# Optimization experiments

Hardware: AMD Instinct MI355X
Metric: run time of the kernel (lower is better)

## Reference

```python
import jax, jax.numpy as jnp
import numpy as np

DIM = 256
HEADS = 8
WIN = 8
N = WIN * WIN          # 64 tokens per window
NW = 1024              # windows per image (256x256 map, 8x8 windows)
BATCH = 4
B_ = BATCH * NW        # 4096
HEAD_DIM = DIM // HEADS


def _relative_position_index():
    # identical to the torch buffer construction in WindowAttention.__init__
    coords = np.stack(np.meshgrid(np.arange(WIN), np.arange(WIN), indexing='ij'))  # [2,W,W]
    flat = coords.reshape(2, -1)                                # [2, N]
    rel = flat[:, :, None] - flat[:, None, :]                   # [2, N, N]
    rel = rel.transpose(1, 2, 0).copy()                         # [N, N, 2]
    rel[:, :, 0] += WIN - 1
    rel[:, :, 1] += WIN - 1
    rel[:, :, 0] *= 2 * WIN - 1
    return jnp.asarray(rel.sum(-1), dtype=jnp.int32)            # [N, N], values in [0, 225)


def setup_inputs() -> dict:
    key = jax.random.key(0)
    ks = jax.random.split(key, 9)
    std = 0.02
    return {
        'x': jax.random.normal(ks[0], (B_, N, DIM), dtype=jnp.float32),
        'mask': jax.random.normal(ks[1], (NW, N, N), dtype=jnp.float32),
        'w_q': jax.random.normal(ks[2], (DIM, DIM), dtype=jnp.float32) * std,
        'b_q': jnp.zeros((DIM,), dtype=jnp.float32),
        'w_kv': jax.random.normal(ks[3], (2 * DIM, DIM), dtype=jnp.float32) * std,
        'b_kv': jnp.zeros((2 * DIM,), dtype=jnp.float32),
        'bias_table': jax.random.normal(ks[4], ((2 * WIN - 1) ** 2, HEADS), dtype=jnp.float32) * std,
        'w_o': jax.random.normal(ks[5], (DIM, DIM), dtype=jnp.float32) * std,
        'b_o': jnp.zeros((DIM,), dtype=jnp.float32),
        'rp_index': _relative_position_index(),
    }


def reference(x, mask, w_q, b_q, w_kv, b_kv, bias_table, w_o, b_o, rp_index):
    Bw, n, c = x.shape
    h, d = HEADS, c // HEADS
    scale = d ** -0.5

    # linear QKV projection (LinearProjection with attn_kv=None)
    q = (x @ w_q.T + b_q).reshape(Bw, n, h, d).transpose(0, 2, 1, 3)      # [B_, H, N, D]
    kv = (x @ w_kv.T + b_kv).reshape(Bw, n, 2, h, d).transpose(2, 0, 3, 1, 4)
    k, v = kv[0], kv[1]                                                    # [B_, H, N, D]

    # scaled QK^T
    attn = jnp.einsum('bhnd,bhmd->bhnm', q * scale, k)                     # [B_, H, N, N]

    # gathered relative position bias (ratio = 1 since attn_kv is None)
    bias = bias_table[rp_index]                                            # [N, N, H]
    attn = attn + bias.transpose(2, 0, 1)[None]                            # broadcast over B_

    # per-window additive mask
    nW = mask.shape[0]
    attn = attn.reshape(Bw // nW, nW, h, n, n) + mask[None, :, None]
    attn = attn.reshape(Bw, h, n, n)

    attn = jax.nn.softmax(attn, axis=-1)

    out = jnp.einsum('bhnm,bhmd->bhnd', attn, v)                           # [B_, H, N, D]
    out = out.transpose(0, 2, 1, 3).reshape(Bw, n, c)
    return out @ w_o.T + b_o
```

## Files before the change

### kernel.cpp

```cpp
#include <hip/hip_runtime.h>
#include <hip/hip_bf16.h>
#include <stdint.h>

typedef __bf16 bf16_t;
typedef bf16_t bf16x8 __attribute__((ext_vector_type(8)));
typedef bf16_t bf16x4 __attribute__((ext_vector_type(4)));
typedef bf16_t bf16x2 __attribute__((ext_vector_type(2)));
typedef float f32x4 __attribute__((ext_vector_type(4)));
typedef uint32_t u32x4 __attribute__((ext_vector_type(4)));

#define WS_WKV_OFF 65536
#define WS_WO_OFF  196608
#define WS_B8_OFF  524288
#define QSCALE 0.17677669529663687f

__global__ __launch_bounds__(256) void prep_kernel(
    const float* __restrict__ wq, const float* __restrict__ wkv,
    const float* __restrict__ wo, const float* __restrict__ bt,
    const int* __restrict__ rp,
    bf16_t* __restrict__ wsq, bf16_t* __restrict__ wskv,
    bf16_t* __restrict__ wso, float* __restrict__ bias8) {
  int t = blockIdx.x * 256 + threadIdx.x;
  if (t < 65536)  wsq[t]  = (bf16_t)(wq[t] * QSCALE);
  if (t < 131072) wskv[t] = (bf16_t)wkv[t];
  if (t < 65536)  wso[t]  = (bf16_t)wo[t];
  if (t < 4096) {
    int idx = rp[t];
#pragma unroll
    for (int h = 0; h < 8; ++h) bias8[h * 4096 + t] = bt[idx * 8 + h];
  }
}

__device__ __forceinline__ bf16x8 xpose_frag(uint32_t e0, uint32_t e1,
                                             uint32_t o0, uint32_t o1,
                                             int ad0, int ad1, bool hi) {
  uint32_t v0e = (uint32_t)__builtin_amdgcn_ds_bpermute(ad0, (int)e0);
  uint32_t v0o = (uint32_t)__builtin_amdgcn_ds_bpermute(ad0, (int)o0);
  uint32_t v1e = (uint32_t)__builtin_amdgcn_ds_bpermute(ad0, (int)e1);
  uint32_t v1o = (uint32_t)__builtin_amdgcn_ds_bpermute(ad0, (int)o1);
  uint32_t v2e = (uint32_t)__builtin_amdgcn_ds_bpermute(ad1, (int)e0);
  uint32_t v2o = (uint32_t)__builtin_amdgcn_ds_bpermute(ad1, (int)o0);
  uint32_t v3e = (uint32_t)__builtin_amdgcn_ds_bpermute(ad1, (int)e1);
  uint32_t v3o = (uint32_t)__builtin_amdgcn_ds_bpermute(ad1, (int)o1);
  u32x4 r;
  r.x = hi ? v0o : v0e;
  r.y = hi ? v1o : v1e;
  r.z = hi ? v2o : v2e;
  r.w = hi ? v3o : v3e;
  return __builtin_bit_cast(bf16x8, r);
}

__device__ __forceinline__ uint32_t pk2(float a, float b) {
  bf16x2 t = {(bf16_t)a, (bf16_t)b};
  return __builtin_bit_cast(uint32_t, t);
}

__global__ __launch_bounds__(512, 4) void win_attn_kernel(
    const float* __restrict__ x, const float* __restrict__ mask,
    const float* __restrict__ bq, const float* __restrict__ bkv,
    const float* __restrict__ bo,
    const bf16_t* __restrict__ wsq, const bf16_t* __restrict__ wskv,
    const bf16_t* __restrict__ wso, const float* __restrict__ bias8,
    float* __restrict__ out) {
  __shared__ bf16_t lds[35328];
  const int b    = blockIdx.x;
  const int tid  = threadIdx.x;
  const int h    = tid >> 6;
  const int lane = tid & 63;
  const int lrow = lane & 15;
  const int lgrp = lane >> 4;
  const bool hi  = (lgrp & 2) != 0;
  const int ad0  = ((((2 * lgrp) & 3) << 4) + lrow) << 2;
  const int ad1  = ((((2 * lgrp + 1) & 3) << 4) + lrow) << 2;
  const f32x4 zf = {0.f, 0.f, 0.f, 0.f};

  {
    const float4* xv = (const float4*)(x + (size_t)b * 16384);
#pragma unroll
    for (int j = 0; j < 8; ++j) {
      int i4 = j * 512 + tid;
      float4 v = xv[i4];
      int e = i4 * 4;
      int r = e >> 8, c = e & 255;
      bf16x4 w = {(bf16_t)v.x, (bf16_t)v.y, (bf16_t)v.z, (bf16_t)v.w};
      *(bf16x4*)(lds + r * 264 + c) = w;
    }
  }
  __syncthreads();

  bf16_t* ldsVt = lds + 16896 + h * 2304;

  {
    const bf16_t* WVh = wskv + (256 + h * 32) * 256;
    float bv0 = bkv[256 + h * 32 + lrow];
    float bv1 = bkv[256 + h * 32 + 16 + lrow];
#pragma unroll
    for (int vh = 0; vh < 2; ++vh) {
      f32x4 av[2][2];
      av[0][0] = av[0][1] = av[1][0] = av[1][1] = zf;
#pragma unroll
      for (int ks = 0; ks < 8; ++ks) {
        bf16x8 xa[2];
#pragma unroll
        for (int i = 0; i < 2; ++i)
          xa[i] = *(const bf16x8*)(lds + ((vh * 2 + i) * 16 + lrow) * 264 + ks * 32 + lgrp * 8);
        bf16x8 wvf[2];
#pragma unroll
        for (int tn = 0; tn < 2; ++tn)
          wvf[tn] = *(const bf16x8*)(WVh + (tn * 16 + lrow) * 256 + ks * 32 + lgrp * 8);
#pragma unroll
        for (int i = 0; i < 2; ++i)
#pragma unroll
          for (int tn = 0; tn < 2; ++tn)
            av[i][tn] = __builtin_amdgcn_mfma_f32_16x16x32_bf16(xa[i], wvf[tn], av[i][tn], 0, 0, 0);
      }
#pragma unroll
      for (int i = 0; i < 2; ++i)
#pragma unroll
        for (int tn = 0; tn < 2; ++tn) {
          float bv = tn ? bv1 : bv0;
          bf16x4 vv;
#pragma unroll
          for (int r = 0; r < 4; ++r) vv[r] = (bf16_t)(av[i][tn][r] + bv);
          *(bf16x4*)(ldsVt + (tn * 16 + lrow) * 72 + (vh * 2 + i) * 16 + lgrp * 4) = vv;
        }
    }
  }

  bf16x8 qb[4], ka[4];
  {
    const bf16_t* WQh = wsq + h * 32 * 256;
#pragma unroll
    for (int qh = 0; qh < 2; ++qh) {
      f32x4 aq[2][2];
      aq[0][0] = aq[0][1] = aq[1][0] = aq[1][1] = zf;
#pragma unroll
      for (int ks = 0; ks < 8; ++ks) {
        bf16x8 xb[2];
#pragma unroll
        for (int i = 0; i < 2; ++i)
          xb[i] = *(const bf16x8*)(lds + ((qh * 2 + i) * 16 + lrow) * 264 + ks * 32 + lgrp * 8);
        bf16x8 wqf[2];
#pragma unroll
        for (int tm = 0; tm < 2; ++tm)
          wqf[tm] = *(const bf16x8*)(WQh + (tm * 16 + lrow) * 256 + ks * 32 + lgrp * 8);
#pragma unroll
        for (int tm = 0; tm < 2; ++tm)
#pragma unroll
          for (int i = 0; i < 2; ++i)
            aq[tm][i] = __builtin_amdgcn_mfma_f32_16x16x32_bf16(wqf[tm], xb[i], aq[tm][i], 0, 0, 0);
      }
      uint32_t pq[2][2][2];
#pragma unroll
      for (int tm = 0; tm < 2; ++tm) {
        float4 b4 = *(const float4*)(bq + h * 32 + tm * 16 + lgrp * 4);
#pragma unroll
        for (int i = 0; i < 2; ++i) {
          pq[tm][i][0] = pk2(aq[tm][i][0] + b4.x * QSCALE, aq[tm][i][1] + b4.y * QSCALE);
          pq[tm][i][1] = pk2(aq[tm][i][2] + b4.z * QSCALE, aq[tm][i][3] + b4.w * QSCALE);
        }
      }
#pragma unroll
      for (int i = 0; i < 2; ++i)
        qb[qh * 2 + i] = xpose_frag(pq[0][i][0], pq[0][i][1], pq[1][i][0], pq[1][i][1], ad0, ad1, hi);
    }
  }
  {
    const bf16_t* WKh = wskv + h * 32 * 256;
#pragma unroll
    for (int kh = 0; kh < 2; ++kh) {
      f32x4 ak2[2][2];
      ak2[0][0] = ak2[0][1] = ak2[1][0] = ak2[1][1] = zf;
#pragma unroll
      for (int ks = 0; ks < 8; ++ks) {
        bf16x8 xb[2];
#pragma unroll
        for (int i = 0; i < 2; ++i)
          xb[i] = *(const bf16x8*)(lds + ((kh * 2 + i) * 16 + lrow) * 264 + ks * 32 + lgrp * 8);
        bf16x8 wkf[2];
#pragma unroll
        for (int tm = 0; tm < 2; ++tm)
          wkf[tm] = *(const bf16x8*)(WKh + (tm * 16 + lrow) * 256 + ks * 32 + lgrp * 8);
#pragma unroll
        for (int tm = 0; tm < 2; ++tm)
#pragma unroll
          for (int i = 0; i < 2; ++i)
            ak2[tm][i] = __builtin_amdgcn_mfma_f32_16x16x32_bf16(wkf[tm], xb[i], ak2[tm][i], 0, 0, 0);
      }
      uint32_t pk[2][2][2];
#pragma unroll
      for (int tm = 0; tm < 2; ++tm) {
        float4 k4 = *(const float4*)(bkv + h * 32 + tm * 16 + lgrp * 4);
#pragma unroll
        for (int i = 0; i < 2; ++i) {
          pk[tm][i][0] = pk2(ak2[tm][i][0] + k4.x, ak2[tm][i][1] + k4.y);
          pk[tm][i][1] = pk2(ak2[tm][i][2] + k4.z, ak2[tm][i][3] + k4.w);
        }
      }
#pragma unroll
      for (int i = 0; i < 2; ++i)
        ka[kh * 2 + i] = xpose_frag(pk[0][i][0], pk[0][i][1], pk[1][i][0], pk[1][i][1], ad0, ad1, hi);
    }
  }

  __syncthreads();

  const float* maskw = mask + (size_t)(b & 1023) * 4096;
  const float* biash = bias8 + h * 4096;
#pragma unroll
  for (int qt = 0; qt < 4; ++qt) {
    f32x4 st[4];
#pragma unroll
    for (int tm = 0; tm < 4; ++tm)
      st[tm] = __builtin_amdgcn_mfma_f32_16x16x32_bf16(ka[tm], qb[qt], zf, 0, 0, 0);
    int q = qt * 16 + lrow;
    float sm = 0.f;
#pragma unroll
    for (int tm = 0; tm < 4; ++tm) {
      int kb = tm * 16 + lgrp * 4;
      float4 mb = *(const float4*)(maskw + q * 64 + kb);
      float4 bb = *(const float4*)(biash + q * 64 + kb);
#pragma unroll
      for (int r = 0; r < 4; ++r) {
        float madd = (r == 0) ? (mb.x + bb.x) : (r == 1) ? (mb.y + bb.y)
                   : (r == 2) ? (mb.z + bb.z) : (mb.w + bb.w);
        float p = __expf(st[tm][r] + madd);
        st[tm][r] = p;
        sm += p;
      }
    }
    sm += __shfl_xor(sm, 16);
    sm += __shfl_xor(sm, 32);
    float rs = 1.0f / sm;
    uint32_t ppk[4][2];
#pragma unroll
    for (int tm = 0; tm < 4; ++tm) {
      ppk[tm][0] = pk2(st[tm][0] * rs, st[tm][1] * rs);
      ppk[tm][1] = pk2(st[tm][2] * rs, st[tm][3] * rs);
    }
    bf16x8 paf[2];
#pragma unroll
    for (int kf = 0; kf < 2; ++kf)
      paf[kf] = xpose_frag(ppk[2 * kf][0], ppk[2 * kf][1],
                           ppk[2 * kf + 1][0], ppk[2 * kf + 1][1], ad0, ad1, hi);
    f32x4 o[2] = {zf, zf};
#pragma unroll
    for (int dt = 0; dt < 2; ++dt)
#pragma unroll
      for (int kf = 0; kf < 2; ++kf) {
        bf16x8 vf = *(const bf16x8*)(ldsVt + (dt * 16 + lrow) * 72 + kf * 32 + lgrp * 8);
        o[dt] = __builtin_amdgcn_mfma_f32_16x16x32_bf16(paf[kf], vf, o[dt], 0, 0, 0);
      }
#pragma unroll
    for (int dt = 0; dt < 2; ++dt)
#pragma unroll
      for (int r = 0; r < 4; ++r)
        lds[(qt * 16 + lgrp * 4 + r) * 264 + h * 32 + dt * 16 + lrow] = (bf16_t)o[dt][r];
  }
  __syncthreads();

  const int nb = h * 32;
  float* outw = out + (size_t)b * 16384;
#pragma unroll
  for (int half = 0; half < 2; ++half) {
    f32x4 oc[2][2];
#pragma unroll
    for (int tm = 0; tm < 2; ++tm)
#pragma unroll
      for (int tn = 0; tn < 2; ++tn) oc[tm][tn] = zf;
#pragma unroll
    for (int ks = 0; ks < 8; ++ks) {
      bf16x8 ao[2];
#pragma unroll
      for (int tm = 0; tm < 2; ++tm)
        ao[tm] = *(const bf16x8*)(lds + ((half * 2 + tm) * 16 + lrow) * 264 + ks * 32 + lgrp * 8);
      bf16x8 bw[2];
#pragma unroll
      for (int tn = 0; tn < 2; ++tn)
        bw[tn] = *(const bf16x8*)(wso + (nb + tn * 16 + lrow) * 256 + ks * 32 + lgrp * 8);
#pragma unroll
      for (int tm = 0; tm < 2; ++tm)
#pragma unroll
        for (int tn = 0; tn < 2; ++tn)
          oc[tm][tn] = __builtin_amdgcn_mfma_f32_16x16x32_bf16(ao[tm], bw[tn], oc[tm][tn], 0, 0, 0);
    }
#pragma unroll
    for (int tn = 0; tn < 2; ++tn) {
      float bov = bo[nb + tn * 16 + lrow];
#pragma unroll
      for (int tm = 0; tm < 2; ++tm)
#pragma unroll
        for (int r = 0; r < 4; ++r)
          outw[((half * 2 + tm) * 16 + lgrp * 4 + r) * 256 + nb + tn * 16 + lrow] =
              oc[tm][tn][r] + bov;
    }
  }
}

extern "C" void kernel_launch(void* const* d_in, const int* in_sizes, int n_in,
                              void* d_out, int out_size, void* d_ws, size_t ws_size,
                              hipStream_t stream) {
  const float* x    = (const float*)d_in[0];
  const float* mask = (const float*)d_in[1];
  const float* wq   = (const float*)d_in[2];
  const float* bq   = (const float*)d_in[3];
  const float* wkv  = (const float*)d_in[4];
  const float* bkv  = (const float*)d_in[5];
  const float* bt   = (const float*)d_in[6];
  const float* wo   = (const float*)d_in[7];
  const float* bo   = (const float*)d_in[8];
  const int*   rp   = (const int*)d_in[9];
  float* out = (float*)d_out;

  bf16_t* wsq  = (bf16_t*)d_ws;
  bf16_t* wskv = wsq + WS_WKV_OFF;
  bf16_t* wso  = wsq + WS_WO_OFF;
  float*  bias8 = (float*)((char*)d_ws + WS_B8_OFF);

  prep_kernel<<<512, 256, 0, stream>>>(wq, wkv, wo, bt, rp, wsq, wskv, wso, bias8);

  win_attn_kernel<<<4096, 512, 0, stream>>>(
      x, mask, bq, bkv, bo, wsq, wskv, wso, bias8, out);
}
```

Measured before the change: 568.5 us.

## Split fused window attention into per-half-head attention and separate out-projection kernels

```diff
diff --git a/kernel.cpp b/kernel.cpp
--- a/kernel.cpp
+++ b/kernel.cpp
@@ -12,6 +12,8 @@
 #define WS_WKV_OFF 65536
 #define WS_WO_OFF  196608
 #define WS_B8_OFF  524288
+#define WS_O_OFF   1048576
+#define WS_NEEDED  (1048576ull + 134217728ull)
 #define QSCALE 0.17677669529663687f
 
 __global__ __launch_bounds__(256) void prep_kernel(
@@ -55,7 +57,260 @@
   return __builtin_bit_cast(uint32_t, t);
 }
 
-__global__ __launch_bounds__(512, 4) void win_attn_kernel(
+__global__ __launch_bounds__(256, 3) void attn_qkv_kernel(
+    const float* __restrict__ x, const float* __restrict__ mask,
+    const float* __restrict__ bq, const float* __restrict__ bkv,
+    const bf16_t* __restrict__ wsq, const bf16_t* __restrict__ wskv,
+    const float* __restrict__ bias8, bf16_t* __restrict__ Ob) {
+  __shared__ bf16_t lds[64 * 264];
+  const int wg   = blockIdx.x;
+  const int b    = wg >> 1;
+  const int half = wg & 1;
+  const int tid  = threadIdx.x;
+  const int h    = half * 4 + (tid >> 6);
+  const int lane = tid & 63;
+  const int lrow = lane & 15;
+  const int lgrp = lane >> 4;
+  const bool hi  = (lgrp & 2) != 0;
+  const int ad0  = ((((2 * lgrp) & 3) << 4) + lrow) << 2;
+  const int ad1  = ((((2 * lgrp + 1) & 3) << 4) + lrow) << 2;
+  const f32x4 zf = {0.f, 0.f, 0.f, 0.f};
+
+  {
+    const float4* xv = (const float4*)(x + (size_t)b * 16384);
+#pragma unroll
+    for (int j = 0; j < 16; ++j) {
+      int i4 = j * 256 + tid;
+      float4 v = xv[i4];
+      int e = i4 * 4;
+      int r = e >> 8, c = e & 255;
+      bf16x4 w = {(bf16_t)v.x, (bf16_t)v.y, (bf16_t)v.z, (bf16_t)v.w};
+      *(bf16x4*)(lds + r * 264 + c) = w;
+    }
+  }
+  __syncthreads();
+
+  bf16x8 vb[2][2];
+  {
+    const bf16_t* WVh = wskv + (256 + h * 32) * 256;
+    float bv0 = bkv[256 + h * 32 + lrow];
+    float bv1 = bkv[256 + h * 32 + 16 + lrow];
+#pragma unroll
+    for (int vh = 0; vh < 2; ++vh) {
+      f32x4 av[2][2];
+      av[0][0] = av[0][1] = av[1][0] = av[1][1] = zf;
+#pragma unroll
+      for (int ks = 0; ks < 8; ++ks) {
+        bf16x8 xa[2];
+#pragma unroll
+        for (int i = 0; i < 2; ++i)
+          xa[i] = *(const bf16x8*)(lds + ((vh * 2 + i) * 16 + lrow) * 264 + ks * 32 + lgrp * 8);
+        bf16x8 wvf[2];
+#pragma unroll
+        for (int tn = 0; tn < 2; ++tn)
+          wvf[tn] = *(const bf16x8*)(WVh + (tn * 16 + lrow) * 256 + ks * 32 + lgrp * 8);
+#pragma unroll
+        for (int i = 0; i < 2; ++i)
+#pragma unroll
+          for (int tn = 0; tn < 2; ++tn)
+            av[i][tn] = __builtin_amdgcn_mfma_f32_16x16x32_bf16(xa[i], wvf[tn], av[i][tn], 0, 0, 0);
+      }
+      uint32_t pkv[2][2][2];
+#pragma unroll
+      for (int i = 0; i < 2; ++i)
+#pragma unroll
+        for (int tn = 0; tn < 2; ++tn) {
+          float bv = tn ? bv1 : bv0;
+          pkv[i][tn][0] = pk2(av[i][tn][0] + bv, av[i][tn][1] + bv);
+          pkv[i][tn][1] = pk2(av[i][tn][2] + bv, av[i][tn][3] + bv);
+        }
+#pragma unroll
+      for (int dt = 0; dt < 2; ++dt)
+        vb[dt][vh] = xpose_frag(pkv[0][dt][0], pkv[0][dt][1],
+                                pkv[1][dt][0], pkv[1][dt][1], ad0, ad1, hi);
+    }
+  }
+
+  bf16x8 qb[4], ka[4];
+  {
+    const bf16_t* WQh = wsq + h * 32 * 256;
+#pragma unroll
+    for (int qh = 0; qh < 2; ++qh) {
+      f32x4 aq[2][2];
+      aq[0][0] = aq[0][1] = aq[1][0] = aq[1][1] = zf;
+#pragma unroll
+      for (int ks = 0; ks < 8; ++ks) {
+        bf16x8 xb[2];
+#pragma unroll
+        for (int i = 0; i < 2; ++i)
+          xb[i] = *(const bf16x8*)(lds + ((qh * 2 + i) * 16 + lrow) * 264 + ks * 32 + lgrp * 8);
+        bf16x8 wqf[2];
+#pragma unroll
+        for (int tm = 0; tm < 2; ++tm)
+          wqf[tm] = *(const bf16x8*)(WQh + (tm * 16 + lrow) * 256 + ks * 32 + lgrp * 8);
+#pragma unroll
+        for (int tm = 0; tm < 2; ++tm)
+#pragma unroll
+          for (int i = 0; i < 2; ++i)
+            aq[tm][i] = __builtin_amdgcn_mfma_f32_16x16x32_bf16(wqf[tm], xb[i], aq[tm][i], 0, 0, 0);
+      }
+      uint32_t pq[2][2][2];
+#pragma unroll
+      for (int tm = 0; tm < 2; ++tm) {
+        float4 b4 = *(const float4*)(bq + h * 32 + tm * 16 + lgrp * 4);
+#pragma unroll
+        for (int i = 0; i < 2; ++i) {
+          pq[tm][i][0] = pk2(aq[tm][i][0] + b4.x * QSCALE, aq[tm][i][1] + b4.y * QSCALE);
+          pq[tm][i][1] = pk2(aq[tm][i][2] + b4.z * QSCALE, aq[tm][i][3] + b4.w * QSCALE);
+        }
+      }
+#pragma unroll
+      for (int i = 0; i < 2; ++i)
+        qb[qh * 2 + i] = xpose_frag(pq[0][i][0], pq[0][i][1], pq[1][i][0], pq[1][i][1], ad0, ad1, hi);
+    }
+  }
+  {
+    const bf16_t* WKh = wskv + h * 32 * 256;
+#pragma unroll
+    for (int kh = 0; kh < 2; ++kh) {
+      f32x4 ak2[2][2];
+      ak2[0][0] = ak2[0][1] = ak2[1][0] = ak2[1][1] = zf;
+#pragma unroll
+      for (int ks = 0; ks < 8; ++ks) {
+        bf16x8 xb[2];
+#pragma unroll
+        for (int i = 0; i < 2; ++i)
+          xb[i] = *(const bf16x8*)(lds + ((kh * 2 + i) * 16 + lrow) * 264 + ks * 32 + lgrp * 8);
+        bf16x8 wkf[2];
+#pragma unroll
+        for (int tm = 0; tm < 2; ++tm)
+          wkf[tm] = *(const bf16x8*)(WKh + (tm * 16 + lrow) * 256 + ks * 32 + lgrp * 8);
+#pragma unroll
+        for (int tm = 0; tm < 2; ++tm)
+#pragma unroll
+          for (int i = 0; i < 2; ++i)
+            ak2[tm][i] = __builtin_amdgcn_mfma_f32_16x16x32_bf16(wkf[tm], xb[i], ak2[tm][i], 0, 0, 0);
+      }
+      uint32_t pkk[2][2][2];
+#pragma unroll
+      for (int tm = 0; tm < 2; ++tm) {
+        float4 k4 = *(const float4*)(bkv + h * 32 + tm * 16 + lgrp * 4);
+#pragma unroll
+        for (int i = 0; i < 2; ++i) {
+          pkk[tm][i][0] = pk2(ak2[tm][i][0] + k4.x, ak2[tm][i][1] + k4.y);
+          pkk[tm][i][1] = pk2(ak2[tm][i][2] + k4.z, ak2[tm][i][3] + k4.w);
+        }
+      }
+#pragma unroll
+      for (int i = 0; i < 2; ++i)
+        ka[kh * 2 + i] = xpose_frag(pkk[0][i][0], pkk[0][i][1], pkk[1][i][0], pkk[1][i][1], ad0, ad1, hi);
+    }
+  }
+
+  const float* maskw = mask + (size_t)(b & 1023) * 4096;
+  const float* biash = bias8 + h * 4096;
+  bf16_t* ow = Ob + (size_t)b * 16384 + h * 32;
+#pragma unroll
+  for (int qt = 0; qt < 4; ++qt) {
+    f32x4 st[4];
+#pragma unroll
+    for (int tm = 0; tm < 4; ++tm)
+      st[tm] = __builtin_amdgcn_mfma_f32_16x16x32_bf16(ka[tm], qb[qt], zf, 0, 0, 0);
+    int q = qt * 16 + lrow;
+    float sm = 0.f;
+#pragma unroll
+    for (int tm = 0; tm < 4; ++tm) {
+      int kb = tm * 16 + lgrp * 4;
+      float4 mb = *(const float4*)(maskw + q * 64 + kb);
+      float4 bb = *(const float4*)(biash + q * 64 + kb);
+#pragma unroll
+      for (int r = 0; r < 4; ++r) {
+        float madd = (r == 0) ? (mb.x + bb.x) : (r == 1) ? (mb.y + bb.y)
+                   : (r == 2) ? (mb.z + bb.z) : (mb.w + bb.w);
+        float p = __expf(st[tm][r] + madd);
+        st[tm][r] = p;
+        sm += p;
+      }
+    }
+    sm += __shfl_xor(sm, 16);
+    sm += __shfl_xor(sm, 32);
+    float rs = 1.0f / sm;
+    uint32_t ppk[4][2];
+#pragma unroll
+    for (int tm = 0; tm < 4; ++tm) {
+      ppk[tm][0] = pk2(st[tm][0] * rs, st[tm][1] * rs);
+      ppk[tm][1] = pk2(st[tm][2] * rs, st[tm][3] * rs);
+    }
+    bf16x8 paf[2];
+#pragma unroll
+    for (int kf = 0; kf < 2; ++kf)
+      paf[kf] = xpose_frag(ppk[2 * kf][0], ppk[2 * kf][1],
+                           ppk[2 * kf + 1][0], ppk[2 * kf + 1][1], ad0, ad1, hi);
+    f32x4 o[2] = {zf, zf};
+#pragma unroll
+    for (int dt = 0; dt < 2; ++dt)
+#pragma unroll
+      for (int kf = 0; kf < 2; ++kf)
+        o[dt] = __builtin_amdgcn_mfma_f32_16x16x32_bf16(paf[kf], vb[dt][kf], o[dt], 0, 0, 0);
+#pragma unroll
+    for (int dt = 0; dt < 2; ++dt)
+#pragma unroll
+      for (int r = 0; r < 4; ++r)
+        ow[(qt * 16 + lgrp * 4 + r) * 256 + dt * 16 + lrow] = (bf16_t)o[dt][r];
+  }
+}
+
+__global__ __launch_bounds__(256, 2) void outproj_kernel(
+    const bf16_t* __restrict__ Ob, const bf16_t* __restrict__ wso,
+    const float* __restrict__ bo, float* __restrict__ out) {
+  __shared__ bf16_t ldsA[64 * 264];
+  const int blk  = blockIdx.x;
+  const size_t t0 = (size_t)blk * 64;
+  const int tid  = threadIdx.x;
+  const int w    = tid >> 6;
+  const int lane = tid & 63;
+  const int lrow = lane & 15;
+  const int lgrp = lane >> 4;
+  const f32x4 zf = {0.f, 0.f, 0.f, 0.f};
+
+  {
+    const bf16_t* src = Ob + t0 * 256;
+#pragma unroll
+    for (int j = 0; j < 8; ++j) {
+      int idx = j * 256 + tid;
+      int e = idx * 8;
+      int r = e >> 8, c = e & 255;
+      *(bf16x8*)(ldsA + r * 264 + c) = *(const bf16x8*)(src + e);
+    }
+  }
+  __syncthreads();
+
+  float* outw = out + t0 * 256;
+#pragma unroll
+  for (int cp = 0; cp < 4; ++cp) {
+    f32x4 acc[4];
+#pragma unroll
+    for (int tn = 0; tn < 4; ++tn) acc[tn] = zf;
+#pragma unroll
+    for (int ks = 0; ks < 8; ++ks) {
+      bf16x8 ao = *(const bf16x8*)(ldsA + (w * 16 + lrow) * 264 + ks * 32 + lgrp * 8);
+#pragma unroll
+      for (int tn = 0; tn < 4; ++tn) {
+        bf16x8 bw = *(const bf16x8*)(wso + (cp * 64 + tn * 16 + lrow) * 256 + ks * 32 + lgrp * 8);
+        acc[tn] = __builtin_amdgcn_mfma_f32_16x16x32_bf16(ao, bw, acc[tn], 0, 0, 0);
+      }
+    }
+#pragma unroll
+    for (int tn = 0; tn < 4; ++tn) {
+      float bov = bo[cp * 64 + tn * 16 + lrow];
+#pragma unroll
+      for (int r = 0; r < 4; ++r)
+        outw[(w * 16 + lgrp * 4 + r) * 256 + cp * 64 + tn * 16 + lrow] = acc[tn][r] + bov;
+    }
+  }
+}
+
+__global__ __launch_bounds__(512, 2) void win_attn_fused(
     const float* __restrict__ x, const float* __restrict__ mask,
     const float* __restrict__ bq, const float* __restrict__ bkv,
     const float* __restrict__ bo,
@@ -73,7 +328,6 @@
   const int ad0  = ((((2 * lgrp) & 3) << 4) + lrow) << 2;
   const int ad1  = ((((2 * lgrp + 1) & 3) << 4) + lrow) << 2;
   const f32x4 zf = {0.f, 0.f, 0.f, 0.f};
-
   {
     const float4* xv = (const float4*)(x + (size_t)b * 16384);
 #pragma unroll
@@ -87,9 +341,7 @@
     }
   }
   __syncthreads();
-
   bf16_t* ldsVt = lds + 16896 + h * 2304;
-
   {
     const bf16_t* WVh = wskv + (256 + h * 32) * 256;
     float bv0 = bkv[256 + h * 32 + lrow];
@@ -126,85 +378,86 @@
         }
     }
   }
-
   bf16x8 qb[4], ka[4];
   {
     const bf16_t* WQh = wsq + h * 32 * 256;
-#pragma unroll
-    for (int qh = 0; qh < 2; ++qh) {
-      f32x4 aq[2][2];
-      aq[0][0] = aq[0][1] = aq[1][0] = aq[1][1] = zf;
-#pragma unroll
-      for (int ks = 0; ks < 8; ++ks) {
-        bf16x8 xb[2];
-#pragma unroll
-        for (int i = 0; i < 2; ++i)
-          xb[i] = *(const bf16x8*)(lds + ((qh * 2 + i) * 16 + lrow) * 264 + ks * 32 + lgrp * 8);
-        bf16x8 wqf[2];
-#pragma unroll
-        for (int tm = 0; tm < 2; ++tm)
-          wqf[tm] = *(const bf16x8*)(WQh + (tm * 16 + lrow) * 256 + ks * 32 + lgrp * 8);
-#pragma unroll
-        for (int tm = 0; tm < 2; ++tm)
-#pragma unroll
-          for (int i = 0; i < 2; ++i)
-            aq[tm][i] = __builtin_amdgcn_mfma_f32_16x16x32_bf16(wqf[tm], xb[i], aq[tm][i], 0, 0, 0);
-      }
-      uint32_t pq[2][2][2];
-#pragma unroll
-      for (int tm = 0; tm < 2; ++tm) {
-        float4 b4 = *(const float4*)(bq + h * 32 + tm * 16 + lgrp * 4);
-#pragma unroll
-        for (int i = 0; i < 2; ++i) {
-          pq[tm][i][0] = pk2(aq[tm][i][0] + b4.x * QSCALE, aq[tm][i][1] + b4.y * QSCALE);
-          pq[tm][i][1] = pk2(aq[tm][i][2] + b4.z * QSCALE, aq[tm][i][3] + b4.w * QSCALE);
-        }
-      }
-#pragma unroll
-      for (int i = 0; i < 2; ++i)
-        qb[qh * 2 + i] = xpose_frag(pq[0][i][0], pq[0][i][1], pq[1][i][0], pq[1][i][1], ad0, ad1, hi);
-    }
+    f32x4 aq[2][4];
+#pragma unroll
+    for (int tm = 0; tm < 2; ++tm)
+#pragma unroll
+      for (int tn = 0; tn < 4; ++tn) aq[tm][tn] = zf;
+#pragma unroll
+    for (int ks = 0; ks < 8; ++ks) {
+      bf16x8 xb[4];
+#pragma unroll
+      for (int tn = 0; tn < 4; ++tn)
+        xb[tn] = *(const bf16x8*)(lds + (tn * 16 + lrow) * 264 + ks * 32 + lgrp * 8);
+      bf16x8 wqf[2];
+#pragma unroll
+      for (int tm = 0; tm < 2; ++tm)
+        wqf[tm] = *(const bf16x8*)(WQh + (tm * 16 + lrow) * 256 + ks * 32 + lgrp * 8);
+#pragma unroll
+      for (int tm = 0; tm < 2; ++tm)
+#pragma unroll
+        for (int tn = 0; tn < 4; ++tn)
+          aq[tm][tn] = __builtin_amdgcn_mfma_f32_16x16x32_bf16(wqf[tm], xb[tn], aq[tm][tn], 0, 0, 0);
+    }
+    uint32_t pkq[2][4][2];
+#pragma unroll
+    for (int tm = 0; tm < 2; ++tm) {
+      float4 b4 = *(const float4*)(bq + h * 32 + tm * 16 + lgrp * 4);
+      float bqa[4] = {b4.x * QSCALE, b4.y * QSCALE, b4.z * QSCALE, b4.w * QSCALE};
+#pragma unroll
+      for (int tn = 0; tn < 4; ++tn)
+#pragma unroll
+        for (int pr = 0; pr < 2; ++pr)
+          pkq[tm][tn][pr] = pk2(aq[tm][tn][2 * pr] + bqa[2 * pr],
+                                aq[tm][tn][2 * pr + 1] + bqa[2 * pr + 1]);
+    }
+#pragma unroll
+    for (int t = 0; t < 4; ++t)
+      qb[t] = xpose_frag(pkq[0][t][0], pkq[0][t][1], pkq[1][t][0], pkq[1][t][1], ad0, ad1, hi);
   }
   {
     const bf16_t* WKh = wskv + h * 32 * 256;
-#pragma unroll
-    for (int kh = 0; kh < 2; ++kh) {
-      f32x4 ak2[2][2];
-      ak2[0][0] = ak2[0][1] = ak2[1][0] = ak2[1][1] = zf;
-#pragma unroll
-      for (int ks = 0; ks < 8; ++ks) {
-        bf16x8 xb[2];
-#pragma unroll
-        for (int i = 0; i < 2; ++i)
-          xb[i] = *(const bf16x8*)(lds + ((kh * 2 + i) * 16 + lrow) * 264 + ks * 32 + lgrp * 8);
-        bf16x8 wkf[2];
-#pragma unroll
-        for (int tm = 0; tm < 2; ++tm)
-          wkf[tm] = *(const bf16x8*)(WKh + (tm * 16 + lrow) * 256 + ks * 32 + lgrp * 8);
-#pragma unroll
-        for (int tm = 0; tm < 2; ++tm)
-#pragma unroll
-          for (int i = 0; i < 2; ++i)
-            ak2[tm][i] = __builtin_amdgcn_mfma_f32_16x16x32_bf16(wkf[tm], xb[i], ak2[tm][i], 0, 0, 0);
-      }
-      uint32_t pk[2][2][2];
-#pragma unroll
-      for (int tm = 0; tm < 2; ++tm) {
-        float4 k4 = *(const float4*)(bkv + h * 32 + tm * 16 + lgrp * 4);
-#pragma unroll
-        for (int i = 0; i < 2; ++i) {
-          pk[tm][i][0] = pk2(ak2[tm][i][0] + k4.x, ak2[tm][i][1] + k4.y);
-          pk[tm][i][1] = pk2(ak2[tm][i][2] + k4.z, ak2[tm][i][3] + k4.w);
-        }
-      }
-#pragma unroll
-      for (int i = 0; i < 2; ++i)
-        ka[kh * 2 + i] = xpose_frag(pk[0][i][0], pk[0][i][1], pk[1][i][0], pk[1][i][1], ad0, ad1, hi);
-    }
-  }
-
+    f32x4 akk[2][4];
+#pragma unroll
+    for (int tm = 0; tm < 2; ++tm)
+#pragma unroll
+      for (int tn = 0; tn < 4; ++tn) akk[tm][tn] = zf;
+#pragma unroll
+    for (int ks = 0; ks < 8; ++ks) {
+      bf16x8 xb[4];
+#pragma unroll
+      for (int tn = 0; tn < 4; ++tn)
+        xb[tn] = *(const bf16x8*)(lds + (tn * 16 + lrow) * 264 + ks * 32 + lgrp * 8);
+      bf16x8 wkf[2];
+#pragma unroll
+      for (int tm = 0; tm < 2; ++tm)
+        wkf[tm] = *(const bf16x8*)(WKh + (tm * 16 + lrow) * 256 + ks * 32 + lgrp * 8);
+#pragma unroll
+      for (int tm = 0; tm < 2; ++tm)
+#pragma unroll
+        for (int tn = 0; tn < 4; ++tn)
+          akk[tm][tn] = __builtin_amdgcn_mfma_f32_16x16x32_bf16(wkf[tm], xb[tn], akk[tm][tn], 0, 0, 0);
+    }
+    uint32_t pkk[2][4][2];
+#pragma unroll
+    for (int tm = 0; tm < 2; ++tm) {
+      float4 k4 = *(const float4*)(bkv + h * 32 + tm * 16 + lgrp * 4);
+      float bka[4] = {k4.x, k4.y, k4.z, k4.w};
+#pragma unroll
+      for (int tn = 0; tn < 4; ++tn)
+#pragma unroll
+        for (int pr = 0; pr < 2; ++pr)
+          pkk[tm][tn][pr] = pk2(akk[tm][tn][2 * pr] + bka[2 * pr],
+                                akk[tm][tn][2 * pr + 1] + bka[2 * pr + 1]);
+    }
+#pragma unroll
+    for (int t = 0; t < 4; ++t)
+      ka[t] = xpose_frag(pkk[0][t][0], pkk[0][t][1], pkk[1][t][0], pkk[1][t][1], ad0, ad1, hi);
+  }
   __syncthreads();
-
   const float* maskw = mask + (size_t)(b & 1023) * 4096;
   const float* biash = bias8 + h * 4096;
 #pragma unroll
@@ -258,7 +511,6 @@
         lds[(qt * 16 + lgrp * 4 + r) * 264 + h * 32 + dt * 16 + lrow] = (bf16_t)o[dt][r];
   }
   __syncthreads();
-
   const int nb = h * 32;
   float* outw = out + (size_t)b * 16384;
 #pragma unroll
@@ -316,9 +568,14 @@
   bf16_t* wskv = wsq + WS_WKV_OFF;
   bf16_t* wso  = wsq + WS_WO_OFF;
   float*  bias8 = (float*)((char*)d_ws + WS_B8_OFF);
+  bf16_t* Ob   = (bf16_t*)((char*)d_ws + WS_O_OFF);
 
   prep_kernel<<<512, 256, 0, stream>>>(wq, wkv, wo, bt, rp, wsq, wskv, wso, bias8);
 
-  win_attn_kernel<<<4096, 512, 0, stream>>>(
-      x, mask, bq, bkv, bo, wsq, wskv, wso, bias8, out);
-}
+  if (ws_size >= WS_NEEDED) {
+    attn_qkv_kernel<<<8192, 256, 0, stream>>>(x, mask, bq, bkv, wsq, wskv, bias8, Ob);
+    outproj_kernel<<<4096, 256, 0, stream>>>(Ob, wso, bo, out);
+  } else {
+    win_attn_fused<<<4096, 512, 0, stream>>>(x, mask, bq, bkv, bo, wsq, wskv, wso, bias8, out);
+  }
+}
```

Result: slower. 790.3 us (+39.0%).

## Use 256-thread blocks with two heads per wave and V kept in registers

Applied to the files above, without the earlier changes.

```diff
diff --git a/kernel.cpp b/kernel.cpp
--- a/kernel.cpp
+++ b/kernel.cpp
@@ -55,17 +55,17 @@
   return __builtin_bit_cast(uint32_t, t);
 }
 
-__global__ __launch_bounds__(512, 4) void win_attn_kernel(
+__global__ __launch_bounds__(256, 3) void win_attn_kernel(
     const float* __restrict__ x, const float* __restrict__ mask,
     const float* __restrict__ bq, const float* __restrict__ bkv,
     const float* __restrict__ bo,
     const bf16_t* __restrict__ wsq, const bf16_t* __restrict__ wskv,
     const bf16_t* __restrict__ wso, const float* __restrict__ bias8,
     float* __restrict__ out) {
-  __shared__ bf16_t lds[35328];
+  __shared__ bf16_t lds[64 * 264];
   const int b    = blockIdx.x;
   const int tid  = threadIdx.x;
-  const int h    = tid >> 6;
+  const int wid  = tid >> 6;
   const int lane = tid & 63;
   const int lrow = lane & 15;
   const int lgrp = lane >> 4;
@@ -77,8 +77,8 @@
   {
     const float4* xv = (const float4*)(x + (size_t)b * 16384);
 #pragma unroll
-    for (int j = 0; j < 8; ++j) {
-      int i4 = j * 512 + tid;
+    for (int j = 0; j < 16; ++j) {
+      int i4 = j * 256 + tid;
       float4 v = xv[i4];
       int e = i4 * 4;
       int r = e >> 8, c = e & 255;
@@ -88,211 +88,221 @@
   }
   __syncthreads();
 
-  bf16_t* ldsVt = lds + 16896 + h * 2304;
-
-  {
-    const bf16_t* WVh = wskv + (256 + h * 32) * 256;
-    float bv0 = bkv[256 + h * 32 + lrow];
-    float bv1 = bkv[256 + h * 32 + 16 + lrow];
-#pragma unroll
-    for (int vh = 0; vh < 2; ++vh) {
-      f32x4 av[2][2];
-      av[0][0] = av[0][1] = av[1][0] = av[1][1] = zf;
-#pragma unroll
-      for (int ks = 0; ks < 8; ++ks) {
-        bf16x8 xa[2];
+  const float* maskw = mask + (size_t)(b & 1023) * 4096;
+  uint32_t opk[2][4][4];
+
+#pragma unroll
+  for (int rd = 0; rd < 2; ++rd) {
+    const int h = wid + rd * 4;
+
+    bf16x8 vb[2][2];
+    {
+      const bf16_t* WVh = wskv + (256 + h * 32) * 256;
+      float bv0 = bkv[256 + h * 32 + lrow];
+      float bv1 = bkv[256 + h * 32 + 16 + lrow];
+#pragma unroll
+      for (int vh = 0; vh < 2; ++vh) {
+        f32x4 av[2][2];
+        av[0][0] = av[0][1] = av[1][0] = av[1][1] = zf;
+#pragma unroll
+        for (int ks = 0; ks < 8; ++ks) {
+          bf16x8 xa[2];
+#pragma unroll
+          for (int i = 0; i < 2; ++i)
+            xa[i] = *(const bf16x8*)(lds + ((vh * 2 + i) * 16 + lrow) * 264 + ks * 32 + lgrp * 8);
+          bf16x8 wvf[2];
+#pragma unroll
+          for (int tn = 0; tn < 2; ++tn)
+            wvf[tn] = *(const bf16x8*)(WVh + (tn * 16 + lrow) * 256 + ks * 32 + lgrp * 8);
+#pragma unroll
+          for (int i = 0; i < 2; ++i)
+#pragma unroll
+            for (int tn = 0; tn < 2; ++tn)
+              av[i][tn] = __builtin_amdgcn_mfma_f32_16x16x32_bf16(xa[i], wvf[tn], av[i][tn], 0, 0, 0);
+        }
+        uint32_t pkv[2][2][2];
 #pragma unroll
         for (int i = 0; i < 2; ++i)
-          xa[i] = *(const bf16x8*)(lds + ((vh * 2 + i) * 16 + lrow) * 264 + ks * 32 + lgrp * 8);
-        bf16x8 wvf[2];
-#pragma unroll
-        for (int tn = 0; tn < 2; ++tn)
-          wvf[tn] = *(const bf16x8*)(WVh + (tn * 16 + lrow) * 256 + ks * 32 + lgrp * 8);
+#pragma unroll
+          for (int tn = 0; tn < 2; ++tn) {
+            float bv = tn ? bv1 : bv0;
+            pkv[i][tn][0] = pk2(av[i][tn][0] + bv, av[i][tn][1] + bv);
+            pkv[i][tn][1] = pk2(av[i][tn][2] + bv, av[i][tn][3] + bv);
+          }
+#pragma unroll
+        for (int dt = 0; dt < 2; ++dt)
+          vb[dt][vh] = xpose_frag(pkv[0][dt][0], pkv[0][dt][1],
+                                  pkv[1][dt][0], pkv[1][dt][1], ad0, ad1, hi);
+      }
+    }
+
+    bf16x8 qb[4], ka[4];
+    {
+      const bf16_t* WQh = wsq + h * 32 * 256;
+#pragma unroll
+      for (int qh = 0; qh < 2; ++qh) {
+        f32x4 aq[2][2];
+        aq[0][0] = aq[0][1] = aq[1][0] = aq[1][1] = zf;
+#pragma unroll
+        for (int ks = 0; ks < 8; ++ks) {
+          bf16x8 xb[2];
+#pragma unroll
+          for (int i = 0; i < 2; ++i)
+            xb[i] = *(const bf16x8*)(lds + ((qh * 2 + i) * 16 + lrow) * 264 + ks * 32 + lgrp * 8);
+          bf16x8 wqf[2];
+#pragma unroll
+          for (int tm = 0; tm < 2; ++tm)
+            wqf[tm] = *(const bf16x8*)(WQh + (tm * 16 + lrow) * 256 + ks * 32 + lgrp * 8);
+#pragma unroll
+          for (int tm = 0; tm < 2; ++tm)
+#pragma unroll
+            for (int i = 0; i < 2; ++i)
+              aq[tm][i] = __builtin_amdgcn_mfma_f32_16x16x32_bf16(wqf[tm], xb[i], aq[tm][i], 0, 0, 0);
+        }
+        uint32_t pq[2][2][2];
+#pragma unroll
+        for (int tm = 0; tm < 2; ++tm) {
+          float4 b4 = *(const float4*)(bq + h * 32 + tm * 16 + lgrp * 4);
+#pragma unroll
+          for (int i = 0; i < 2; ++i) {
+            pq[tm][i][0] = pk2(aq[tm][i][0] + b4.x * QSCALE, aq[tm][i][1] + b4.y * QSCALE);
+            pq[tm][i][1] = pk2(aq[tm][i][2] + b4.z * QSCALE, aq[tm][i][3] + b4.w * QSCALE);
+          }
+        }
 #pragma unroll
         for (int i = 0; i < 2; ++i)
-#pragma unroll
-          for (int tn = 0; tn < 2; ++tn)
-            av[i][tn] = __builtin_amdgcn_mfma_f32_16x16x32_bf16(xa[i], wvf[tn], av[i][tn], 0, 0, 0);
-      }
-#pragma unroll
-      for (int i = 0; i < 2; ++i)
-#pragma unroll
-        for (int tn = 0; tn < 2; ++tn) {
-          float bv = tn ? bv1 : bv0;
-          bf16x4 vv;
-#pragma unroll
-          for (int r = 0; r < 4; ++r) vv[r] = (bf16_t)(av[i][tn][r] + bv);
-          *(bf16x4*)(ldsVt + (tn * 16 + lrow) * 72 + (vh * 2 + i) * 16 + lgrp * 4) = vv;
-        }
-    }
-  }
-
-  bf16x8 qb[4], ka[4];
-  {
-    const bf16_t* WQh = wsq + h * 32 * 256;
-#pragma unroll
-    for (int qh = 0; qh < 2; ++qh) {
-      f32x4 aq[2][2];
-      aq[0][0] = aq[0][1] = aq[1][0] = aq[1][1] = zf;
-#pragma unroll
-      for (int ks = 0; ks < 8; ++ks) {
-        bf16x8 xb[2];
+          qb[qh * 2 + i] = xpose_frag(pq[0][i][0], pq[0][i][1], pq[1][i][0], pq[1][i][1], ad0, ad1, hi);
+      }
+    }
+    {
+      const bf16_t* WKh = wskv + h * 32 * 256;
+#pragma unroll
+      for (int kh = 0; kh < 2; ++kh) {
+        f32x4 ak2[2][2];
+        ak2[0][0] = ak2[0][1] = ak2[1][0] = ak2[1][1] = zf;
+#pragma unroll
+        for (int ks = 0; ks < 8; ++ks) {
+          bf16x8 xb[2];
+#pragma unroll
+          for (int i = 0; i < 2; ++i)
+            xb[i] = *(const bf16x8*)(lds + ((kh * 2 + i) * 16 + lrow) * 264 + ks * 32 + lgrp * 8);
+          bf16x8 wkf[2];
+#pragma unroll
+          for (int tm = 0; tm < 2; ++tm)
+            wkf[tm] = *(const bf16x8*)(WKh + (tm * 16 + lrow) * 256 + ks * 32 + lgrp * 8);
+#pragma unroll
+          for (int tm = 0; tm < 2; ++tm)
+#pragma unroll
+            for (int i = 0; i < 2; ++i)
+              ak2[tm][i] = __builtin_amdgcn_mfma_f32_16x16x32_bf16(wkf[tm], xb[i], ak2[tm][i], 0, 0, 0);
+        }
+        uint32_t pkk[2][2][2];
+#pragma unroll
+        for (int tm = 0; tm < 2; ++tm) {
+          float4 k4 = *(const float4*)(bkv + h * 32 + tm * 16 + lgrp * 4);
+#pragma unroll
+          for (int i = 0; i < 2; ++i) {
+            pkk[tm][i][0] = pk2(ak2[tm][i][0] + k4.x, ak2[tm][i][1] + k4.y);
+            pkk[tm][i][1] = pk2(ak2[tm][i][2] + k4.z, ak2[tm][i][3] + k4.w);
+          }
+        }
 #pragma unroll
         for (int i = 0; i < 2; ++i)
-          xb[i] = *(const bf16x8*)(lds + ((qh * 2 + i) * 16 + lrow) * 264 + ks * 32 + lgrp * 8);
-        bf16x8 wqf[2];
-#pragma unroll
-        for (int tm = 0; tm < 2; ++tm)
-          wqf[tm] = *(const bf16x8*)(WQh + (tm * 16 + lrow) * 256 + ks * 32 + lgrp * 8);
-#pragma unroll
-        for (int tm = 0; tm < 2; ++tm)
-#pragma unroll
-          for (int i = 0; i < 2; ++i)
-            aq[tm][i] = __builtin_amdgcn_mfma_f32_16x16x32_bf16(wqf[tm], xb[i], aq[tm][i], 0, 0, 0);
-      }
-      uint32_t pq[2][2][2];
-#pragma unroll
-      for (int tm = 0; tm < 2; ++tm) {
-        float4 b4 = *(const float4*)(bq + h * 32 + tm * 16 + lgrp * 4);
-#pragma unroll
-        for (int i = 0; i < 2; ++i) {
-          pq[tm][i][0] = pk2(aq[tm][i][0] + b4.x * QSCALE, aq[tm][i][1] + b4.y * QSCALE);
-          pq[tm][i][1] = pk2(aq[tm][i][2] + b4.z * QSCALE, aq[tm][i][3] + b4.w * QSCALE);
-        }
-      }
-#pragma unroll
-      for (int i = 0; i < 2; ++i)
-        qb[qh * 2 + i] = xpose_frag(pq[0][i][0], pq[0][i][1], pq[1][i][0], pq[1][i][1], ad0, ad1, hi);
-    }
-  }
-  {
-    const bf16_t* WKh = wskv + h * 32 * 256;
-#pragma unroll
-    for (int kh = 0; kh < 2; ++kh) {
-      f32x4 ak2[2][2];
-      ak2[0][0] = ak2[0][1] = ak2[1][0] = ak2[1][1] = zf;
-#pragma unroll
-      for (int ks = 0; ks < 8; ++ks) {
-        bf16x8 xb[2];
-#pragma unroll
-        for (int i = 0; i < 2; ++i)
-          xb[i] = *(const bf16x8*)(lds + ((kh * 2 + i) * 16 + lrow) * 264 + ks * 32 + lgrp * 8);
-        bf16x8 wkf[2];
-#pragma unroll
-        for (int tm = 0; tm < 2; ++tm)
-          wkf[tm] = *(const bf16x8*)(WKh + (tm * 16 + lrow) * 256 + ks * 32 + lgrp * 8);
-#pragma unroll
-        for (int tm = 0; tm < 2; ++tm)
-#pragma unroll
-          for (int i = 0; i < 2; ++i)
-            ak2[tm][i] = __builtin_amdgcn_mfma_f32_16x16x32_bf16(wkf[tm], xb[i], ak2[tm][i], 0, 0, 0);
-      }
-      uint32_t pk[2][2][2];
-#pragma unroll
-      for (int tm = 0; tm < 2; ++tm) {
-        float4 k4 = *(const float4*)(bkv + h * 32 + tm * 16 + lgrp * 4);
-#pragma unroll
-        for (int i = 0; i < 2; ++i) {
-          pk[tm][i][0] = pk2(ak2[tm][i][0] + k4.x, ak2[tm][i][1] + k4.y);
-          pk[tm][i][1] = pk2(ak2[tm][i][2] + k4.z, ak2[tm][i][3] + k4.w);
-        }
-      }
-#pragma unroll
-      for (int i = 0; i < 2; ++i)
-        ka[kh * 2 + i] = xpose_frag(pk[0][i][0], pk[0][i][1], pk[1][i][0], pk[1][i][1], ad0, ad1, hi);
+          ka[kh * 2 + i] = xpose_frag(pkk[0][i][0], pkk[0][i][1], pkk[1][i][0], pkk[1][i][1], ad0, ad1, hi);
+      }
+    }
+
+    const float* biash = bias8 + h * 4096;
+#pragma unroll
+    for (int qt = 0; qt < 4; ++qt) {
+      f32x4 st[4];
+#pragma unroll
+      for (int tm = 0; tm < 4; ++tm)
+        st[tm] = __builtin_amdgcn_mfma_f32_16x16x32_bf16(ka[tm], qb[qt], zf, 0, 0, 0);
+      int q = qt * 16 + lrow;
+      float sm = 0.f;
+#pragma unroll
+      for (int tm = 0; tm < 4; ++tm) {
+        int kb = tm * 16 + lgrp * 4;
+        float4 mb = *(const float4*)(maskw + q * 64 + kb);
+        float4 bb = *(const float4*)(biash + q * 64 + kb);
+#pragma unroll
+        for (int r = 0; r < 4; ++r) {
+          float madd = (r == 0) ? (mb.x + bb.x) : (r == 1) ? (mb.y + bb.y)
+                     : (r == 2) ? (mb.z + bb.z) : (mb.w + bb.w);
+          float p = __expf(st[tm][r] + madd);
+          st[tm][r] = p;
+          sm += p;
+        }
+      }
+      sm += __shfl_xor(sm, 16);
+      sm += __shfl_xor(sm, 32);
+      float rs = 1.0f / sm;
+      uint32_t ppk[4][2];
+#pragma unroll
+      for (int tm = 0; tm < 4; ++tm) {
+        ppk[tm][0] = pk2(st[tm][0] * rs, st[tm][1] * rs);
+        ppk[tm][1] = pk2(st[tm][2] * rs, st[tm][3] * rs);
+      }
+      bf16x8 paf[2];
+#pragma unroll
+      for (int kf = 0; kf < 2; ++kf)
+        paf[kf] = xpose_frag(ppk[2 * kf][0], ppk[2 * kf][1],
+                             ppk[2 * kf + 1][0], ppk[2 * kf + 1][1], ad0, ad1, hi);
+      f32x4 o[2] = {zf, zf};
+#pragma unroll
+      for (int dt = 0; dt < 2; ++dt)
+#pragma unroll
+        for (int kf = 0; kf < 2; ++kf)
+          o[dt] = __builtin_amdgcn_mfma_f32_16x16x32_bf16(paf[kf], vb[dt][kf], o[dt], 0, 0, 0);
+#pragma unroll
+      for (int dt = 0; dt < 2; ++dt) {
+        opk[rd][qt][dt * 2]     = pk2(o[dt][0], o[dt][1]);
+        opk[rd][qt][dt * 2 + 1] = pk2(o[dt][2], o[dt][3]);
+      }
     }
   }
 
   __syncthreads();
-
-  const float* maskw = mask + (size_t)(b & 1023) * 4096;
-  const float* biash = bias8 + h * 4096;
-#pragma unroll
-  for (int qt = 0; qt < 4; ++qt) {
-    f32x4 st[4];
-#pragma unroll
-    for (int tm = 0; tm < 4; ++tm)
-      st[tm] = __builtin_amdgcn_mfma_f32_16x16x32_bf16(ka[tm], qb[qt], zf, 0, 0, 0);
-    int q = qt * 16 + lrow;
-    float sm = 0.f;
-#pragma unroll
-    for (int tm = 0; tm < 4; ++tm) {
-      int kb = tm * 16 + lgrp * 4;
-      float4 mb = *(const float4*)(maskw + q * 64 + kb);
-      float4 bb = *(const float4*)(biash + q * 64 + kb);
-#pragma unroll
-      for (int r = 0; r < 4; ++r) {
-        float madd = (r == 0) ? (mb.x + bb.x) : (r == 1) ? (mb.y + bb.y)
-                   : (r == 2) ? (mb.z + bb.z) : (mb.w + bb.w);
-        float p = __expf(st[tm][r] + madd);
-        st[tm][r] = p;
-        sm += p;
-      }
-    }
-    sm += __shfl_xor(sm, 16);
-    sm += __shfl_xor(sm, 32);
-    float rs = 1.0f / sm;
-    uint32_t ppk[4][2];
-#pragma unroll
-    for (int tm = 0; tm < 4; ++tm) {
-      ppk[tm][0] = pk2(st[tm][0] * rs, st[tm][1] * rs);
-      ppk[tm][1] = pk2(st[tm][2] * rs, st[tm][3] * rs);
-    }
-    bf16x8 paf[2];
-#pragma unroll
-    for (int kf = 0; kf < 2; ++kf)
-      paf[kf] = xpose_frag(ppk[2 * kf][0], ppk[2 * kf][1],
-                           ppk[2 * kf + 1][0], ppk[2 * kf + 1][1], ad0, ad1, hi);
-    f32x4 o[2] = {zf, zf};
-#pragma unroll
-    for (int dt = 0; dt < 2; ++dt)
-#pragma unroll
-      for (int kf = 0; kf < 2; ++kf) {
-        bf16x8 vf = *(const bf16x8*)(ldsVt + (dt * 16 + lrow) * 72 + kf * 32 + lgrp * 8);
-        o[dt] = __builtin_amdgcn_mfma_f32_16x16x32_bf16(paf[kf], vf, o[dt], 0, 0, 0);
-      }
-#pragma unroll
-    for (int dt = 0; dt < 2; ++dt)
+#pragma unroll
+  for (int rd = 0; rd < 2; ++rd) {
+    int col0 = (wid + rd * 4) * 32;
+#pragma unroll
+    for (int qt = 0; qt < 4; ++qt)
+#pragma unroll
+      for (int dt = 0; dt < 2; ++dt)
+#pragma unroll
+        for (int pr = 0; pr < 2; ++pr) {
+          bf16x2 t = __builtin_bit_cast(bf16x2, opk[rd][qt][dt * 2 + pr]);
+          int row = qt * 16 + lgrp * 4 + 2 * pr;
+          int col = col0 + dt * 16 + lrow;
+          lds[row * 264 + col] = t[0];
+          lds[(row + 1) * 264 + col] = t[1];
+        }
+  }
+  __syncthreads();
+
+  float* outw = out + (size_t)b * 16384;
+#pragma unroll
+  for (int cp = 0; cp < 4; ++cp) {
+    f32x4 acc[4];
+#pragma unroll
+    for (int tn = 0; tn < 4; ++tn) acc[tn] = zf;
+#pragma unroll
+    for (int ks = 0; ks < 8; ++ks) {
+      bf16x8 ao = *(const bf16x8*)(lds + (wid * 16 + lrow) * 264 + ks * 32 + lgrp * 8);
+#pragma unroll
+      for (int tn = 0; tn < 4; ++tn) {
+        bf16x8 bw = *(const bf16x8*)(wso + (cp * 64 + tn * 16 + lrow) * 256 + ks * 32 + lgrp * 8);
+        acc[tn] = __builtin_amdgcn_mfma_f32_16x16x32_bf16(ao, bw, acc[tn], 0, 0, 0);
+      }
+    }
+#pragma unroll
+    for (int tn = 0; tn < 4; ++tn) {
+      float bov = bo[cp * 64 + tn * 16 + lrow];
 #pragma unroll
       for (int r = 0; r < 4; ++r)
-        lds[(qt * 16 + lgrp * 4 + r) * 264 + h * 32 + dt * 16 + lrow] = (bf16_t)o[dt][r];
-  }
-  __syncthreads();
-
-  const int nb = h * 32;
-  float* outw = out + (size_t)b * 16384;
-#pragma unroll
-  for (int half = 0; half < 2; ++half) {
-    f32x4 oc[2][2];
-#pragma unroll
-    for (int tm = 0; tm < 2; ++tm)
-#pragma unroll
-      for (int tn = 0; tn < 2; ++tn) oc[tm][tn] = zf;
-#pragma unroll
-    for (int ks = 0; ks < 8; ++ks) {
-      bf16x8 ao[2];
-#pragma unroll
-      for (int tm = 0; tm < 2; ++tm)
-        ao[tm] = *(const bf16x8*)(lds + ((half * 2 + tm) * 16 + lrow) * 264 + ks * 32 + lgrp * 8);
-      bf16x8 bw[2];
-#pragma unroll
-      for (int tn = 0; tn < 2; ++tn)
-        bw[tn] = *(const bf16x8*)(wso + (nb + tn * 16 + lrow) * 256 + ks * 32 + lgrp * 8);
-#pragma unroll
-      for (int tm = 0; tm < 2; ++tm)
-#pragma unroll
-        for (int tn = 0; tn < 2; ++tn)
-          oc[tm][tn] = __builtin_amdgcn_mfma_f32_16x16x32_bf16(ao[tm], bw[tn], oc[tm][tn], 0, 0, 0);
-    }
-#pragma unroll
-    for (int tn = 0; tn < 2; ++tn) {
-      float bov = bo[nb + tn * 16 + lrow];
-#pragma unroll
-      for (int tm = 0; tm < 2; ++tm)
-#pragma unroll
-        for (int r = 0; r < 4; ++r)
-          outw[((half * 2 + tm) * 16 + lgrp * 4 + r) * 256 + nb + tn * 16 + lrow] =
-              oc[tm][tn][r] + bov;
+        outw[(wid * 16 + lgrp * 4 + r) * 256 + cp * 64 + tn * 16 + lrow] = acc[tn][r] + bov;
     }
   }
 }
@@ -319,6 +329,6 @@
 
   prep_kernel<<<512, 256, 0, stream>>>(wq, wkv, wo, bt, rp, wsq, wskv, wso, bias8);
 
-  win_attn_kernel<<<4096, 512, 0, stream>>>(
+  win_attn_kernel<<<4096, 256, 0, stream>>>(
       x, mask, bq, bkv, bo, wsq, wskv, wso, bias8, out);
 }
```

Measured after the change: 969.3 us. +70.5%, slower.
